# Optimization experiments

Hardware: AMD Instinct MI355X
Metric: run time of the kernel (lower is better)

Reference implementation:

```python
import jax, jax.numpy as jnp
import numpy as np

D = 2          # qudit dimension
L = 22         # number of qudits; state length = D**L = 4194304
INDEX = tuple(range(L))  # rotation applied on every qudit (angle[i] indexed by qudit position)

# Generator S = Sx(j=0, k=1) on a D-level system: |0><1| + |1><0|
def _make_S():
    S = np.zeros((D, D), dtype=np.complex64)
    S[0, 1] = 1.0
    S[1, 0] = 1.0
    return jnp.asarray(S)


def setup_inputs() -> dict:
    key = jax.random.key(0)
    k1, k2, k3 = jax.random.split(key, 3)
    n = D ** L
    x_real = jax.random.normal(k1, (n,), dtype=jnp.float32)
    x_imag = jax.random.normal(k2, (n,), dtype=jnp.float32)
    angle = jax.random.uniform(k3, (L,), dtype=jnp.float32)
    return {"x_real": x_real, "x_imag": x_imag, "angle": angle}


def reference(x_real, x_imag, angle):
    # U = kron_i expm(-0.5j * angle[i] * S)  (identity on qudits not in INDEX),
    # applied as U @ x. Instead of materializing the D^L x D^L sparse unitary,
    # apply each single-qudit gate by contracting axis i of the reshaped state,
    # which is exactly the same linear map.
    S = _make_S()
    psi = (x_real + 1j * x_imag).astype(jnp.complex64).reshape((D,) * L)
    for i in range(L):
        if i in INDEX:
            M = jax.scipy.linalg.expm((-0.5j) * angle[i].astype(jnp.complex64) * S)
            # contract qudit axis i: psi'[..., a, ...] = sum_b M[a,b] psi[..., b, ...]
            psi = jnp.moveaxis(jnp.tensordot(M, psi, axes=([1], [i])), 0, i)
        # else: identity, nothing to do
    out = psi.reshape(-1)
    return jnp.stack([out.real, out.imag])  # (2, D**L) float32
```

## Files before the change

kernel.cpp:

```cpp
#include <hip/hip_runtime.h>


constexpr int NTOT = 1 << 22;

__device__ __forceinline__ void rotg(float& ar, float& ai, float& br, float& bi,
                                     float c, float s) {
    float t0 = ar, t1 = ai, t2 = br, t3 = bi;
    ar = fmaf(c, t0,  s * t3);
    ai = fmaf(c, t1, -s * t2);
    br = fmaf(c, t2,  s * t1);
    bi = fmaf(c, t3, -s * t0);
}

__device__ __forceinline__ void build_cs(const float* __restrict__ ang,
                                         float* cs_c, float* cs_s, int t) {
    if (t < 22) {
        float a = 0.5f * ang[21 - t];
        cs_c[t] = cosf(a);
        cs_s[t] = sinf(a);
    }
}

__device__ __forceinline__ int padslot(int i) { return i + (i >> 4) + (i >> 8); }

__global__ __launch_bounds__(256, 4) void rgate_low(const float* __restrict__ xr,
                                                    const float* __restrict__ xi,
                                                    const float* __restrict__ ang,
                                                    float* __restrict__ out) {
    __shared__ float2 sv[4368];
    __shared__ float cs_c[22], cs_s[22];
    const int t  = threadIdx.x;
    const int g0 = blockIdx.x << 12;

    build_cs(ang, cs_c, cs_s, t);

    float ar[16], ai[16];
    const float* xrp = xr + g0 + t;
    const float* xip = xi + g0 + t;
    #pragma unroll
    for (int j = 0; j < 16; ++j) {
        ar[j] = xrp[j << 8];
        ai[j] = xip[j << 8];
    }
    __syncthreads();

    #pragma unroll
    for (int b = 0; b < 4; ++b) {
        const int m = 1 << b;
        const float c = cs_c[8 + b], s = cs_s[8 + b];
        #pragma unroll
        for (int j = 0; j < 16; ++j)
            if (!(j & m)) rotg(ar[j], ai[j], ar[j | m], ai[j | m], c, s);
    }
    #pragma unroll
    for (int j = 0; j < 16; ++j)
        sv[padslot(t + (j << 8))] = make_float2(ar[j], ai[j]);
    __syncthreads();

    {
        const int base2 = (t & 15) + ((t >> 4) << 8);
        #pragma unroll
        for (int j = 0; j < 16; ++j) {
            float2 v = sv[padslot(base2 + (j << 4))];
            ar[j] = v.x; ai[j] = v.y;
        }
        #pragma unroll
        for (int b = 0; b < 4; ++b) {
            const int m = 1 << b;
            const float c = cs_c[4 + b], s = cs_s[4 + b];
            #pragma unroll
            for (int j = 0; j < 16; ++j)
                if (!(j & m)) rotg(ar[j], ai[j], ar[j | m], ai[j | m], c, s);
        }
        #pragma unroll
        for (int j = 0; j < 16; ++j)
            sv[padslot(base2 + (j << 4))] = make_float2(ar[j], ai[j]);
    }
    __syncthreads();

    {
        const int base3 = t << 4;
        #pragma unroll
        for (int j = 0; j < 16; ++j) {
            float2 v = sv[padslot(base3 + j)];
            ar[j] = v.x; ai[j] = v.y;
        }
        #pragma unroll
        for (int b = 0; b < 4; ++b) {
            const int m = 1 << b;
            const float c = cs_c[b], s = cs_s[b];
            #pragma unroll
            for (int j = 0; j < 16; ++j)
                if (!(j & m)) rotg(ar[j], ai[j], ar[j | m], ai[j | m], c, s);
        }
        float4* orp = (float4*)(out + g0 + base3);
        float4* oip = (float4*)(out + NTOT + g0 + base3);
        #pragma unroll
        for (int q = 0; q < 4; ++q) {
            orp[q] = make_float4(ar[4*q], ar[4*q+1], ar[4*q+2], ar[4*q+3]);
            oip[q] = make_float4(ai[4*q], ai[4*q+1], ai[4*q+2], ai[4*q+3]);
        }
    }
}

__global__ __launch_bounds__(256) void rgate_mid(const float* __restrict__ ang,
                                                 float* __restrict__ out) {
    __shared__ float2 sv[2048];
    __shared__ float cs_c[22], cs_s[22];
    const int t    = threadIdx.x;
    const int lane = t & 63, w = t >> 6;
    const int bid  = blockIdx.x;
    const int base = ((bid >> 6) << 17) + ((bid & 63) << 6) + lane;
    float* outr = out;
    float* outi = out + NTOT;

    build_cs(ang, cs_c, cs_s, t);

    float ar[8], ai[8];
    #pragma unroll
    for (int j = 0; j < 8; ++j) {
        const int g = base + ((j | (w << 3)) << 12);
        ar[j] = outr[g]; ai[j] = outi[g];
    }
    __syncthreads();

    #pragma unroll
    for (int b = 0; b < 3; ++b) {
        const int m = 1 << b;
        const float c = cs_c[12 + b], s = cs_s[12 + b];
        #pragma unroll
        for (int j = 0; j < 8; ++j)
            if (!(j & m)) rotg(ar[j], ai[j], ar[j | m], ai[j | m], c, s);
    }
    #pragma unroll
    for (int j = 0; j < 8; ++j)
        sv[((j | (w << 3)) << 6) + lane] = make_float2(ar[j], ai[j]);
    __syncthreads();

    #pragma unroll
    for (int j = 0; j < 8; ++j) {
        const int h = ((j & 3) << 3) | (w << 1) | (j >> 2);
        float2 v = sv[(h << 6) + lane];
        ar[j] = v.x; ai[j] = v.y;
    }
    #pragma unroll
    for (int b = 0; b < 2; ++b) {
        const int m = 1 << b;
        const float c = cs_c[15 + b], s = cs_s[15 + b];
        #pragma unroll
        for (int j = 0; j < 8; ++j)
            if (!(j & m)) rotg(ar[j], ai[j], ar[j | m], ai[j | m], c, s);
    }
    #pragma unroll
    for (int j = 0; j < 8; ++j) {
        const int h = ((j & 3) << 3) | (w << 1) | (j >> 2);
        const int g = base + (h << 12);
        outr[g] = ar[j]; outi[g] = ai[j];
    }
}

__global__ __launch_bounds__(256) void rgate_high(const float* __restrict__ ang,
                                                  float* __restrict__ out) {
    __shared__ float2 sv[2048];
    __shared__ float cs_c[22], cs_s[22];
    const int t    = threadIdx.x;
    const int lane = t & 63, w = t >> 6;
    const int base = (blockIdx.x << 6) + lane;
    float* outr = out;
    float* outi = out + NTOT;

    build_cs(ang, cs_c, cs_s, t);

    float ar[8], ai[8];
    #pragma unroll
    for (int j = 0; j < 8; ++j) {
        const int g = ((j | (w << 3)) << 17) + base;
        ar[j] = outr[g]; ai[j] = outi[g];
    }
    __syncthreads();

    #pragma unroll
    for (int b = 0; b < 3; ++b) {
        const int m = 1 << b;
        const float c = cs_c[17 + b], s = cs_s[17 + b];
        #pragma unroll
        for (int j = 0; j < 8; ++j)
            if (!(j & m)) rotg(ar[j], ai[j], ar[j | m], ai[j | m], c, s);
    }
    #pragma unroll
    for (int j = 0; j < 8; ++j)
        sv[((j | (w << 3)) << 6) + lane] = make_float2(ar[j], ai[j]);
    __syncthreads();

    #pragma unroll
    for (int j = 0; j < 8; ++j) {
        const int u = ((j & 3) << 3) | (w << 1) | (j >> 2);
        float2 v = sv[(u << 6) + lane];
        ar[j] = v.x; ai[j] = v.y;
    }
    #pragma unroll
    for (int b = 0; b < 2; ++b) {
        const int m = 1 << b;
        const float c = cs_c[20 + b], s = cs_s[20 + b];
        #pragma unroll
        for (int j = 0; j < 8; ++j)
            if (!(j & m)) rotg(ar[j], ai[j], ar[j | m], ai[j | m], c, s);
    }
    #pragma unroll
    for (int j = 0; j < 8; ++j) {
        const int u = ((j & 3) << 3) | (w << 1) | (j >> 2);
        const int g = (u << 17) + base;
        outr[g] = ar[j]; outi[g] = ai[j];
    }
}

extern "C" void kernel_launch(void* const* d_in, const int* in_sizes, int n_in,
                              void* d_out, int out_size, void* d_ws, size_t ws_size,
                              hipStream_t stream) {
    const float* xr  = (const float*)d_in[0];
    const float* xi  = (const float*)d_in[1];
    const float* ang = (const float*)d_in[2];
    float* out = (float*)d_out;

    rgate_low<<<1024, 256, 0, stream>>>(xr, xi, ang, out);
    rgate_mid<<<2048, 256, 0, stream>>>(ang, out);
    rgate_high<<<2048, 256, 0, stream>>>(ang, out);
}
```

Measured before the change: 113.0 us.

## Fuse qudit rotations into two passes with 13-bit and 9-bit tiles

```diff
diff --git a/kernel.cpp b/kernel.cpp
--- a/kernel.cpp
+++ b/kernel.cpp
@@ -12,205 +12,185 @@
     bi = fmaf(c, t3, -s * t0);
 }
 
-__device__ __forceinline__ void build_cs(const float* __restrict__ ang,
-                                         float* cs_c, float* cs_s, int t) {
-    if (t < 22) {
-        float a = 0.5f * ang[21 - t];
-        cs_c[t] = cosf(a);
-        cs_s[t] = sinf(a);
-    }
-}
-
-__device__ __forceinline__ int padslot(int i) { return i + (i >> 4) + (i >> 8); }
-
-__global__ __launch_bounds__(256, 4) void rgate_low(const float* __restrict__ xr,
-                                                    const float* __restrict__ xi,
-                                                    const float* __restrict__ ang,
-                                                    float* __restrict__ out) {
-    __shared__ float2 sv[4368];
-    __shared__ float cs_c[22], cs_s[22];
+__device__ __forceinline__ void rot4(float4& ar, float4& ai, float4& br, float4& bi,
+                                     float c, float s) {
+    rotg(ar.x, ai.x, br.x, bi.x, c, s);
+    rotg(ar.y, ai.y, br.y, bi.y, c, s);
+    rotg(ar.z, ai.z, br.z, bi.z, c, s);
+    rotg(ar.w, ai.w, br.w, bi.w, c, s);
+}
+
+__device__ __forceinline__ int slotA(int i) { return i + 2 * (i >> 4) + 4 * (i >> 9); }
+
+__device__ __forceinline__ int slotB(int h, int lq) {
+    const int z = (h ^ (h >> 3) ^ (h >> 6)) & 7;
+    return h * 18 + ((lq + 2 * z) & 15);
+}
+
+__global__ __launch_bounds__(256) void rgate_lo(const float* __restrict__ xr,
+                                                const float* __restrict__ xi,
+                                                const float* __restrict__ ang,
+                                                float* __restrict__ out) {
+    extern __shared__ float4 svraw[];
+    float2* sv = (float2*)svraw;
+    __shared__ float csc[22], css[22];
     const int t  = threadIdx.x;
-    const int g0 = blockIdx.x << 12;
-
-    build_cs(ang, cs_c, cs_s, t);
-
-    float ar[16], ai[16];
-    const float* xrp = xr + g0 + t;
-    const float* xip = xi + g0 + t;
-    #pragma unroll
-    for (int j = 0; j < 16; ++j) {
-        ar[j] = xrp[j << 8];
-        ai[j] = xip[j << 8];
-    }
-    __syncthreads();
-
-    #pragma unroll
-    for (int b = 0; b < 4; ++b) {
+    const int g0 = blockIdx.x << 13;
+    if (t < 22) { float a = 0.5f * ang[21 - t]; csc[t] = cosf(a); css[t] = sinf(a); }
+
+    float ar[32], ai[32];
+    #pragma unroll
+    for (int j = 0; j < 32; ++j) {
+        ar[j] = xr[g0 + t + (j << 8)];
+        ai[j] = xi[g0 + t + (j << 8)];
+    }
+    __syncthreads();
+
+    #pragma unroll
+    for (int b = 0; b < 5; ++b) {
         const int m = 1 << b;
-        const float c = cs_c[8 + b], s = cs_s[8 + b];
-        #pragma unroll
-        for (int j = 0; j < 16; ++j)
+        const float c = csc[8 + b], s = css[8 + b];
+        #pragma unroll
+        for (int j = 0; j < 32; ++j)
             if (!(j & m)) rotg(ar[j], ai[j], ar[j | m], ai[j | m], c, s);
     }
     #pragma unroll
-    for (int j = 0; j < 16; ++j)
-        sv[padslot(t + (j << 8))] = make_float2(ar[j], ai[j]);
-    __syncthreads();
-
-    {
-        const int base2 = (t & 15) + ((t >> 4) << 8);
-        #pragma unroll
-        for (int j = 0; j < 16; ++j) {
-            float2 v = sv[padslot(base2 + (j << 4))];
+    for (int j = 0; j < 32; ++j)
+        sv[slotA(t + (j << 8))] = make_float2(ar[j], ai[j]);
+    __syncthreads();
+
+    {
+        const int r = t & 31, hi = t >> 5;
+        #pragma unroll
+        for (int j = 0; j < 32; ++j) {
+            float2 v = sv[slotA(r + (j << 5) + (hi << 10))];
             ar[j] = v.x; ai[j] = v.y;
         }
         #pragma unroll
-        for (int b = 0; b < 4; ++b) {
-            const int m = 1 << b;
-            const float c = cs_c[4 + b], s = cs_s[4 + b];
-            #pragma unroll
-            for (int j = 0; j < 16; ++j)
+        for (int b = 0; b < 3; ++b) {
+            const int m = 1 << b;
+            const float c = csc[5 + b], s = css[5 + b];
+            #pragma unroll
+            for (int j = 0; j < 32; ++j)
                 if (!(j & m)) rotg(ar[j], ai[j], ar[j | m], ai[j | m], c, s);
         }
         #pragma unroll
-        for (int j = 0; j < 16; ++j)
-            sv[padslot(base2 + (j << 4))] = make_float2(ar[j], ai[j]);
-    }
-    __syncthreads();
-
-    {
-        const int base3 = t << 4;
-        #pragma unroll
-        for (int j = 0; j < 16; ++j) {
-            float2 v = sv[padslot(base3 + j)];
-            ar[j] = v.x; ai[j] = v.y;
-        }
-        #pragma unroll
-        for (int b = 0; b < 4; ++b) {
-            const int m = 1 << b;
-            const float c = cs_c[b], s = cs_s[b];
-            #pragma unroll
-            for (int j = 0; j < 16; ++j)
+        for (int j = 0; j < 32; ++j)
+            sv[slotA(r + (j << 5) + (hi << 10))] = make_float2(ar[j], ai[j]);
+    }
+    __syncthreads();
+
+    {
+        #pragma unroll
+        for (int p = 0; p < 16; ++p) {
+            float4 v = *(const float4*)&sv[slotA((t << 5) + 2 * p)];
+            ar[2 * p]     = v.x; ai[2 * p]     = v.y;
+            ar[2 * p + 1] = v.z; ai[2 * p + 1] = v.w;
+        }
+        #pragma unroll
+        for (int b = 0; b < 5; ++b) {
+            const int m = 1 << b;
+            const float c = csc[b], s = css[b];
+            #pragma unroll
+            for (int j = 0; j < 32; ++j)
                 if (!(j & m)) rotg(ar[j], ai[j], ar[j | m], ai[j | m], c, s);
         }
-        float4* orp = (float4*)(out + g0 + base3);
-        float4* oip = (float4*)(out + NTOT + g0 + base3);
-        #pragma unroll
-        for (int q = 0; q < 4; ++q) {
-            orp[q] = make_float4(ar[4*q], ar[4*q+1], ar[4*q+2], ar[4*q+3]);
-            oip[q] = make_float4(ai[4*q], ai[4*q+1], ai[4*q+2], ai[4*q+3]);
-        }
-    }
-}
-
-__global__ __launch_bounds__(256) void rgate_mid(const float* __restrict__ ang,
-                                                 float* __restrict__ out) {
-    __shared__ float2 sv[2048];
-    __shared__ float cs_c[22], cs_s[22];
-    const int t    = threadIdx.x;
-    const int lane = t & 63, w = t >> 6;
-    const int bid  = blockIdx.x;
-    const int base = ((bid >> 6) << 17) + ((bid & 63) << 6) + lane;
-    float* outr = out;
-    float* outi = out + NTOT;
-
-    build_cs(ang, cs_c, cs_s, t);
-
-    float ar[8], ai[8];
+        float4* orp = (float4*)(out + g0 + (t << 5));
+        float4* oip = (float4*)(out + NTOT + g0 + (t << 5));
+        #pragma unroll
+        for (int e = 0; e < 8; ++e) {
+            orp[e] = make_float4(ar[4*e], ar[4*e+1], ar[4*e+2], ar[4*e+3]);
+            oip[e] = make_float4(ai[4*e], ai[4*e+1], ai[4*e+2], ai[4*e+3]);
+        }
+    }
+}
+
+__global__ __launch_bounds__(256) void rgate_hi(const float* __restrict__ ang,
+                                                float* __restrict__ out) {
+    extern __shared__ float4 svraw[];
+    float2* sv = (float2*)svraw;
+    __shared__ float csc[22], css[22];
+    const int t     = threadIdx.x;
+    const int q     = t >> 2;
+    const int lq    = (t & 3) << 2;
+    const int cbase = (blockIdx.x << 4) + lq;
+    if (t < 22) { float a = 0.5f * ang[21 - t]; csc[t] = cosf(a); css[t] = sinf(a); }
+
+    float4 vr[8], vi[8];
     #pragma unroll
     for (int j = 0; j < 8; ++j) {
-        const int g = base + ((j | (w << 3)) << 12);
-        ar[j] = outr[g]; ai[j] = outi[g];
+        const int g = ((q + (j << 6)) << 13) + cbase;
+        vr[j] = *(const float4*)(out + g);
+        vi[j] = *(const float4*)(out + NTOT + g);
     }
     __syncthreads();
 
     #pragma unroll
     for (int b = 0; b < 3; ++b) {
         const int m = 1 << b;
-        const float c = cs_c[12 + b], s = cs_s[12 + b];
+        const float c = csc[19 + b], s = css[19 + b];
         #pragma unroll
         for (int j = 0; j < 8; ++j)
-            if (!(j & m)) rotg(ar[j], ai[j], ar[j | m], ai[j | m], c, s);
-    }
-    #pragma unroll
-    for (int j = 0; j < 8; ++j)
-        sv[((j | (w << 3)) << 6) + lane] = make_float2(ar[j], ai[j]);
-    __syncthreads();
-
+            if (!(j & m)) rot4(vr[j], vi[j], vr[j | m], vi[j | m], c, s);
+    }
     #pragma unroll
     for (int j = 0; j < 8; ++j) {
-        const int h = ((j & 3) << 3) | (w << 1) | (j >> 2);
-        float2 v = sv[(h << 6) + lane];
-        ar[j] = v.x; ai[j] = v.y;
-    }
-    #pragma unroll
-    for (int b = 0; b < 2; ++b) {
-        const int m = 1 << b;
-        const float c = cs_c[15 + b], s = cs_s[15 + b];
-        #pragma unroll
-        for (int j = 0; j < 8; ++j)
-            if (!(j & m)) rotg(ar[j], ai[j], ar[j | m], ai[j | m], c, s);
-    }
-    #pragma unroll
-    for (int j = 0; j < 8; ++j) {
-        const int h = ((j & 3) << 3) | (w << 1) | (j >> 2);
-        const int g = base + (h << 12);
-        outr[g] = ar[j]; outi[g] = ai[j];
-    }
-}
-
-__global__ __launch_bounds__(256) void rgate_high(const float* __restrict__ ang,
-                                                  float* __restrict__ out) {
-    __shared__ float2 sv[2048];
-    __shared__ float cs_c[22], cs_s[22];
-    const int t    = threadIdx.x;
-    const int lane = t & 63, w = t >> 6;
-    const int base = (blockIdx.x << 6) + lane;
-    float* outr = out;
-    float* outi = out + NTOT;
-
-    build_cs(ang, cs_c, cs_s, t);
-
-    float ar[8], ai[8];
-    #pragma unroll
-    for (int j = 0; j < 8; ++j) {
-        const int g = ((j | (w << 3)) << 17) + base;
-        ar[j] = outr[g]; ai[j] = outi[g];
-    }
-    __syncthreads();
-
-    #pragma unroll
-    for (int b = 0; b < 3; ++b) {
-        const int m = 1 << b;
-        const float c = cs_c[17 + b], s = cs_s[17 + b];
-        #pragma unroll
-        for (int j = 0; j < 8; ++j)
-            if (!(j & m)) rotg(ar[j], ai[j], ar[j | m], ai[j | m], c, s);
-    }
-    #pragma unroll
-    for (int j = 0; j < 8; ++j)
-        sv[((j | (w << 3)) << 6) + lane] = make_float2(ar[j], ai[j]);
-    __syncthreads();
-
-    #pragma unroll
-    for (int j = 0; j < 8; ++j) {
-        const int u = ((j & 3) << 3) | (w << 1) | (j >> 2);
-        float2 v = sv[(u << 6) + lane];
-        ar[j] = v.x; ai[j] = v.y;
-    }
-    #pragma unroll
-    for (int b = 0; b < 2; ++b) {
-        const int m = 1 << b;
-        const float c = cs_c[20 + b], s = cs_s[20 + b];
-        #pragma unroll
-        for (int j = 0; j < 8; ++j)
-            if (!(j & m)) rotg(ar[j], ai[j], ar[j | m], ai[j | m], c, s);
-    }
-    #pragma unroll
-    for (int j = 0; j < 8; ++j) {
-        const int u = ((j & 3) << 3) | (w << 1) | (j >> 2);
-        const int g = (u << 17) + base;
-        outr[g] = ar[j]; outi[g] = ai[j];
+        const int sb = slotB(q + (j << 6), lq);
+        *(float4*)&sv[sb]     = make_float4(vr[j].x, vi[j].x, vr[j].y, vi[j].y);
+        *(float4*)&sv[sb + 2] = make_float4(vr[j].z, vi[j].z, vr[j].w, vi[j].w);
+    }
+    __syncthreads();
+
+    {
+        const int hbase = (q & 7) + ((q >> 3) << 6);
+        #pragma unroll
+        for (int j = 0; j < 8; ++j) {
+            const int sb = slotB(hbase + (j << 3), lq);
+            float4 v0 = *(const float4*)&sv[sb];
+            float4 v1 = *(const float4*)&sv[sb + 2];
+            vr[j] = make_float4(v0.x, v0.z, v1.x, v1.z);
+            vi[j] = make_float4(v0.y, v0.w, v1.y, v1.w);
+        }
+        #pragma unroll
+        for (int b = 0; b < 3; ++b) {
+            const int m = 1 << b;
+            const float c = csc[16 + b], s = css[16 + b];
+            #pragma unroll
+            for (int j = 0; j < 8; ++j)
+                if (!(j & m)) rot4(vr[j], vi[j], vr[j | m], vi[j | m], c, s);
+        }
+        #pragma unroll
+        for (int j = 0; j < 8; ++j) {
+            const int sb = slotB(hbase + (j << 3), lq);
+            *(float4*)&sv[sb]     = make_float4(vr[j].x, vi[j].x, vr[j].y, vi[j].y);
+            *(float4*)&sv[sb + 2] = make_float4(vr[j].z, vi[j].z, vr[j].w, vi[j].w);
+        }
+    }
+    __syncthreads();
+
+    {
+        #pragma unroll
+        for (int j = 0; j < 8; ++j) {
+            const int sb = slotB(j + (q << 3), lq);
+            float4 v0 = *(const float4*)&sv[sb];
+            float4 v1 = *(const float4*)&sv[sb + 2];
+            vr[j] = make_float4(v0.x, v0.z, v1.x, v1.z);
+            vi[j] = make_float4(v0.y, v0.w, v1.y, v1.w);
+        }
+        #pragma unroll
+        for (int b = 0; b < 3; ++b) {
+            const int m = 1 << b;
+            const float c = csc[13 + b], s = css[13 + b];
+            #pragma unroll
+            for (int j = 0; j < 8; ++j)
+                if (!(j & m)) rot4(vr[j], vi[j], vr[j | m], vi[j | m], c, s);
+        }
+        #pragma unroll
+        for (int j = 0; j < 8; ++j) {
+            const int g = ((j + (q << 3)) << 13) + cbase;
+            *(float4*)(out + g)        = vr[j];
+            *(float4*)(out + NTOT + g) = vi[j];
+        }
     }
 }
 
@@ -222,7 +202,6 @@
     const float* ang = (const float*)d_in[2];
     float* out = (float*)d_out;
 
-    rgate_low<<<1024, 256, 0, stream>>>(xr, xi, ang, out);
-    rgate_mid<<<2048, 256, 0, stream>>>(ang, out);
-    rgate_high<<<2048, 256, 0, stream>>>(ang, out);
-}
+    rgate_lo<<<512, 256, 74192, stream>>>(xr, xi, ang, out);
+    rgate_hi<<<512, 256, 73728, stream>>>(ang, out);
+}
```

Result: slower. 116.4 us (+3.0%).

## Fuse mid and high qubit passes into one large-LDS kernel

Applied to the files above, without the earlier changes.

```diff
diff --git a/kernel.cpp b/kernel.cpp
--- a/kernel.cpp
+++ b/kernel.cpp
@@ -12,15 +12,6 @@
     bi = fmaf(c, t3, -s * t0);
 }
 
-__device__ __forceinline__ void build_cs(const float* __restrict__ ang,
-                                         float* cs_c, float* cs_s, int t) {
-    if (t < 22) {
-        float a = 0.5f * ang[21 - t];
-        cs_c[t] = cosf(a);
-        cs_s[t] = sinf(a);
-    }
-}
-
 __device__ __forceinline__ int padslot(int i) { return i + (i >> 4) + (i >> 8); }
 
 __global__ __launch_bounds__(256, 4) void rgate_low(const float* __restrict__ xr,
@@ -32,7 +23,7 @@
     const int t  = threadIdx.x;
     const int g0 = blockIdx.x << 12;
 
-    build_cs(ang, cs_c, cs_s, t);
+    if (t < 22) { float a = 0.5f * ang[21 - t]; cs_c[t] = cosf(a); cs_s[t] = sinf(a); }
 
     float ar[16], ai[16];
     const float* xrp = xr + g0 + t;
@@ -103,114 +94,84 @@
     }
 }
 
-__global__ __launch_bounds__(256) void rgate_mid(const float* __restrict__ ang,
-                                                 float* __restrict__ out) {
-    __shared__ float2 sv[2048];
-    __shared__ float cs_c[22], cs_s[22];
+__global__ __launch_bounds__(1024, 4) void rgate_hi(const float* __restrict__ ang,
+                                                    float* __restrict__ out) {
+    extern __shared__ float lds[];
+    float* sr = lds;
+    float* si = lds + 17408;
+    __shared__ float csc[22], css[22];
     const int t    = threadIdx.x;
-    const int lane = t & 63, w = t >> 6;
-    const int bid  = blockIdx.x;
-    const int base = ((bid >> 6) << 17) + ((bid & 63) << 6) + lane;
-    float* outr = out;
-    float* outi = out + NTOT;
+    const int c    = t & 15;
+    const int q    = t >> 4;
+    const int col0 = (blockIdx.x << 4) + c;
 
-    build_cs(ang, cs_c, cs_s, t);
+    if (t < 22) { float a = 0.5f * ang[21 - t]; csc[t] = cosf(a); css[t] = sinf(a); }
 
-    float ar[8], ai[8];
+    float vr[16], vi[16];
     #pragma unroll
-    for (int j = 0; j < 8; ++j) {
-        const int g = base + ((j | (w << 3)) << 12);
-        ar[j] = outr[g]; ai[j] = outi[g];
+    for (int j = 0; j < 16; ++j) {
+        const int g = ((q + (j << 6)) << 12) + col0;
+        vr[j] = out[g]; vi[j] = out[NTOT + g];
     }
     __syncthreads();
 
     #pragma unroll
-    for (int b = 0; b < 3; ++b) {
+    for (int b = 0; b < 4; ++b) {
         const int m = 1 << b;
-        const float c = cs_c[12 + b], s = cs_s[12 + b];
+        const float cc = csc[18 + b], ss = css[18 + b];
         #pragma unroll
-        for (int j = 0; j < 8; ++j)
-            if (!(j & m)) rotg(ar[j], ai[j], ar[j | m], ai[j | m], c, s);
+        for (int j = 0; j < 16; ++j)
+            if (!(j & m)) rotg(vr[j], vi[j], vr[j | m], vi[j | m], cc, ss);
     }
     #pragma unroll
-    for (int j = 0; j < 8; ++j)
-        sv[((j | (w << 3)) << 6) + lane] = make_float2(ar[j], ai[j]);
-    __syncthreads();
-
-    #pragma unroll
-    for (int j = 0; j < 8; ++j) {
-        const int h = ((j & 3) << 3) | (w << 1) | (j >> 2);
-        float2 v = sv[(h << 6) + lane];
-        ar[j] = v.x; ai[j] = v.y;
-    }
-    #pragma unroll
-    for (int b = 0; b < 2; ++b) {
-        const int m = 1 << b;
-        const float c = cs_c[15 + b], s = cs_s[15 + b];
-        #pragma unroll
-        for (int j = 0; j < 8; ++j)
-            if (!(j & m)) rotg(ar[j], ai[j], ar[j | m], ai[j | m], c, s);
-    }
-    #pragma unroll
-    for (int j = 0; j < 8; ++j) {
-        const int h = ((j & 3) << 3) | (w << 1) | (j >> 2);
-        const int g = base + (h << 12);
-        outr[g] = ar[j]; outi[g] = ai[j];
-    }
-}
-
-__global__ __launch_bounds__(256) void rgate_high(const float* __restrict__ ang,
-                                                  float* __restrict__ out) {
-    __shared__ float2 sv[2048];
-    __shared__ float cs_c[22], cs_s[22];
-    const int t    = threadIdx.x;
-    const int lane = t & 63, w = t >> 6;
-    const int base = (blockIdx.x << 6) + lane;
-    float* outr = out;
-    float* outi = out + NTOT;
-
-    build_cs(ang, cs_c, cs_s, t);
-
-    float ar[8], ai[8];
-    #pragma unroll
-    for (int j = 0; j < 8; ++j) {
-        const int g = ((j | (w << 3)) << 17) + base;
-        ar[j] = outr[g]; ai[j] = outi[g];
+    for (int j = 0; j < 16; ++j) {
+        const int h = q + (j << 6);
+        sr[h * 17 + c] = vr[j]; si[h * 17 + c] = vi[j];
     }
     __syncthreads();
 
-    #pragma unroll
-    for (int b = 0; b < 3; ++b) {
-        const int m = 1 << b;
-        const float c = cs_c[17 + b], s = cs_s[17 + b];
+    {
+        const int hb = (q & 3) + ((q >> 2) << 6);
         #pragma unroll
-        for (int j = 0; j < 8; ++j)
-            if (!(j & m)) rotg(ar[j], ai[j], ar[j | m], ai[j | m], c, s);
+        for (int j = 0; j < 16; ++j) {
+            const int h = hb + (j << 2);
+            vr[j] = sr[h * 17 + c]; vi[j] = si[h * 17 + c];
+        }
+        #pragma unroll
+        for (int b = 0; b < 4; ++b) {
+            const int m = 1 << b;
+            const float cc = csc[14 + b], ss = css[14 + b];
+            #pragma unroll
+            for (int j = 0; j < 16; ++j)
+                if (!(j & m)) rotg(vr[j], vi[j], vr[j | m], vi[j | m], cc, ss);
+        }
+        #pragma unroll
+        for (int j = 0; j < 16; ++j) {
+            const int h = hb + (j << 2);
+            sr[h * 17 + c] = vr[j]; si[h * 17 + c] = vi[j];
+        }
     }
-    #pragma unroll
-    for (int j = 0; j < 8; ++j)
-        sv[((j | (w << 3)) << 6) + lane] = make_float2(ar[j], ai[j]);
     __syncthreads();
 
-    #pragma unroll
-    for (int j = 0; j < 8; ++j) {
-        const int u = ((j & 3) << 3) | (w << 1) | (j >> 2);
-        float2 v = sv[(u << 6) + lane];
-        ar[j] = v.x; ai[j] = v.y;
-    }
-    #pragma unroll
-    for (int b = 0; b < 2; ++b) {
-        const int m = 1 << b;
-        const float c = cs_c[20 + b], s = cs_s[20 + b];
+    {
         #pragma unroll
-        for (int j = 0; j < 8; ++j)
-            if (!(j & m)) rotg(ar[j], ai[j], ar[j | m], ai[j | m], c, s);
-    }
-    #pragma unroll
-    for (int j = 0; j < 8; ++j) {
-        const int u = ((j & 3) << 3) | (w << 1) | (j >> 2);
-        const int g = (u << 17) + base;
-        outr[g] = ar[j]; outi[g] = ai[j];
+        for (int j = 0; j < 16; ++j) {
+            const int h = (q << 4) + j;
+            vr[j] = sr[h * 17 + c]; vi[j] = si[h * 17 + c];
+        }
+        #pragma unroll
+        for (int b = 0; b < 2; ++b) {
+            const int m = 1 << b;
+            const float cc = csc[12 + b], ss = css[12 + b];
+            #pragma unroll
+            for (int j = 0; j < 16; ++j)
+                if (!(j & m)) rotg(vr[j], vi[j], vr[j | m], vi[j | m], cc, ss);
+        }
+        #pragma unroll
+        for (int j = 0; j < 16; ++j) {
+            const int g = (((q << 4) + j) << 12) + col0;
+            out[g] = vr[j]; out[NTOT + g] = vi[j];
+        }
     }
 }
 
@@ -222,7 +183,10 @@
     const float* ang = (const float*)d_in[2];
     float* out = (float*)d_out;
 
+    static_assert(2 * 1024 * 17 * 4 == 139264, "");
+    hipFuncSetAttribute((const void*)rgate_hi,
+                        hipFuncAttributeMaxDynamicSharedMemorySize, 139264);
+
     rgate_low<<<1024, 256, 0, stream>>>(xr, xi, ang, out);
-    rgate_mid<<<2048, 256, 0, stream>>>(ang, out);
-    rgate_high<<<2048, 256, 0, stream>>>(ang, out);
+    rgate_hi<<<256, 1024, 139264, stream>>>(ang, out);
 }
```

Measured after the change: 113.2 us. No clear change (+0.2%).
